# Kernel tuning notes

Hardware: AMD Instinct MI355X
Metric: run time of the kernel (lower is better)

Reference implementation:

```python
import jax, jax.numpy as jnp
import numpy as np

LN_EPS = 1e-5


def setup_inputs() -> dict:
    key = jax.random.key(0)
    k1, k2, k3 = jax.random.split(key, 3)
    B, L, D = 8, 2048, 512
    K, Dc = 8192, 16
    x = jax.random.normal(k1, (B, L, D), dtype=jnp.float32)
    # xavier_uniform for Linear(dim -> codebook_dim), weight shape (Dc, D)
    bound = float(np.sqrt(6.0 / (D + Dc)))
    proj_weight = jax.random.uniform(k2, (Dc, D), dtype=jnp.float32, minval=-bound, maxval=bound)
    codebook = jax.random.normal(k3, (K, Dc), dtype=jnp.float32)
    return {"x": x, "proj_weight": proj_weight, "codebook": codebook}


def reference(x, proj_weight, codebook):
    # random projection: (B,L,D) @ (D,Dc) -> (B,L,Dc)
    h = jnp.einsum("bld,cd->blc", x, proj_weight)
    # LayerNorm over last dim, no affine params
    mu = jnp.mean(h, axis=-1, keepdims=True)
    var = jnp.mean(jnp.square(h - mu), axis=-1, keepdims=True)
    h = (h - mu) / jnp.sqrt(var + LN_EPS)
    # squared-distance via dot-product decomposition; avoids (B,L,K,Dc) blowup.
    # argmin of ||h - c||^2 == argmin of ||h - c|| (sqrt is monotone).
    h2 = jnp.sum(jnp.square(h), axis=-1, keepdims=True)        # (B,L,1)
    c2 = jnp.sum(jnp.square(codebook), axis=-1)                # (K,)
    dots = jnp.einsum("blc,kc->blk", h, codebook)              # (B,L,K)
    dist2 = h2 - 2.0 * dots + c2                               # (B,L,K)
    codes = jnp.argmin(dist2, axis=-1)                         # (B,L) int
    return codes
```

## Files before the change

kernel.cpp:

```cpp
#include <hip/hip_runtime.h>
#include <math.h>

#define LN_EPS 1e-5f

typedef _Float16 f16;
typedef _Float16 f16x8 __attribute__((ext_vector_type(8)));
typedef _Float16 f16x2 __attribute__((ext_vector_type(2)));
typedef float f32x4 __attribute__((ext_vector_type(4)));

constexpr int DC = 16;
constexpr int K = 8192;
constexpr int NTOK = 16384;
constexpr int D = 512;
constexpr float SCALE = 16384.f;
constexpr float EPS_S = LN_EPS * SCALE * SCALE;

static __device__ __forceinline__ f16x8 mk8(f16x2 a, f16x2 b, f16x2 c,
                                            f16x2 d) {
  union {
    f16x2 p[4];
    f16x8 v;
  } u;
  u.p[0] = a;
  u.p[1] = b;
  u.p[2] = c;
  u.p[3] = d;
  return u.v;
}

static __device__ __forceinline__ void hilo2(float f0, float f1, f16x2& ph,
                                             f16x2& pl) {
  float h0 = __uint_as_float(__float_as_uint(f0) & 0xFFFFE000u);
  float h1 = __uint_as_float(__float_as_uint(f1) & 0xFFFFE000u);
  ph = __builtin_bit_cast(f16x2, __builtin_amdgcn_cvt_pkrtz(h0, h1));
  pl = __builtin_bit_cast(f16x2,
                          __builtin_amdgcn_cvt_pkrtz(f0 - h0, f1 - h1));
}

__global__ __launch_bounds__(256) void prep(const float* __restrict__ cb,
                                            const float* __restrict__ wq,
                                            f16* __restrict__ cbA,
                                            float* __restrict__ c2s,
                                            f16* __restrict__ wAf) {
  const int tid = threadIdx.x;

  if (blockIdx.x == K / 64) {
#pragma unroll
    for (int i = 0; i < 8; ++i) {
      int slot = tid + 256 * i;
      int tile = slot >> 6;
      int l = slot & 63;
      int g = l >> 4;
      int col = l & 15;
      int doff = (g & 1) * 8;
      const float* wp = wq + (size_t)col * D + tile * 16 + doff;
      f32x4 u0 = *(const f32x4*)wp;
      f32x4 u1 = *(const f32x4*)(wp + 4);
      f16x2 ph[4], pl[4];
      hilo2(u0[0] * 64.f, u0[1] * 64.f, ph[0], pl[0]);
      hilo2(u0[2] * 64.f, u0[3] * 64.f, ph[1], pl[1]);
      hilo2(u1[0] * 64.f, u1[1] * 64.f, ph[2], pl[2]);
      hilo2(u1[2] * 64.f, u1[3] * 64.f, ph[3], pl[3]);
      f16x8 hi = mk8(ph[0], ph[1], ph[2], ph[3]);
      f16x8 lo = mk8(pl[0], pl[1], pl[2], pl[3]);
      *(f16x8*)(wAf + (size_t)slot * 8) = (g < 2) ? hi : lo;
    }
    return;
  }

  const int ti = tid >> 6;
  const int l = tid & 63;
  const int ct = blockIdx.x * 4 + ti;
  const int code = ct * 16 + (l & 15);
  const int g = l >> 4;

  const float* row = cb + (size_t)code * DC + (g & 1) * 8;
  f32x4 v0 = *(const f32x4*)row;
  f32x4 v1 = *(const f32x4*)(row + 4);
  f16x2 ph[4], pl[4];
  hilo2(v0[0] * -128.f, v0[1] * -128.f, ph[0], pl[0]);
  hilo2(v0[2] * -128.f, v0[3] * -128.f, ph[1], pl[1]);
  hilo2(v1[0] * -128.f, v1[1] * -128.f, ph[2], pl[2]);
  hilo2(v1[2] * -128.f, v1[3] * -128.f, ph[3], pl[3]);
  f16x8 hi = mk8(ph[0], ph[1], ph[2], ph[3]);
  f16x8 lo = mk8(pl[0], pl[1], pl[2], pl[3]);
  *(f16x8*)(cbA + ((size_t)ct * 64 + l) * 8) = (g < 2) ? hi : lo;

  if (g == 0) {
    const f32x4* rw = (const f32x4*)(cb + (size_t)code * DC);
    f32x4 a0 = rw[0], a1 = rw[1], a2 = rw[2], a3 = rw[3];
    float s = 0.f;
#pragma unroll
    for (int p = 0; p < 4; ++p)
      s += a0[p] * a0[p] + a1[p] * a1[p] + a2[p] * a2[p] + a3[p] * a3[p];
    c2s[code] = (s + 16.5f) * SCALE;
  }
}

__global__ __launch_bounds__(1024, 8) void fused(
    const float* __restrict__ x, const float* __restrict__ cb,
    const f16* __restrict__ cbA, const float* __restrict__ c2s,
    const f16* __restrict__ wAf, int* __restrict__ out) {
  __shared__ float comb[16 * 16 * 20];
  __shared__ float hsm[32 * 20];
  __shared__ float fin_d[16][32];
  __shared__ int fin_t[16][32];

  const int tid = threadIdx.x;
  const int w = tid >> 6;
  const int lane = tid & 63;
  const int g = lane >> 4;
  const int col = lane & 15;
  const int doff = (g & 1) * 8;
  const int tb = blockIdx.x * 32;

  const int j = w & 1;
  const int dq8 = w >> 1;

  const float* xrow = x + (size_t)(tb + j * 16 + col) * D + dq8 * 64 + doff;
  f32x4 xu0[4], xu1[4];
#pragma unroll
  for (int st = 0; st < 4; ++st) {
    xu0[st] = *(const f32x4*)(xrow + st * 16);
    xu1[st] = *(const f32x4*)(xrow + st * 16 + 4);
  }
  f16x8 aw[4];
#pragma unroll
  for (int st = 0; st < 4; ++st)
    aw[st] = *(const f16x8*)(wAf + ((size_t)(dq8 * 4 + st) * 64 + lane) * 8);

  f32x4 acc = {0.f, 0.f, 0.f, 0.f};
#pragma unroll
  for (int st = 0; st < 4; ++st) {
    f16x2 ph[4], pl[4];
    hilo2(xu0[st][0] * 256.f, xu0[st][1] * 256.f, ph[0], pl[0]);
    hilo2(xu0[st][2] * 256.f, xu0[st][3] * 256.f, ph[1], pl[1]);
    hilo2(xu1[st][0] * 256.f, xu1[st][1] * 256.f, ph[2], pl[2]);
    hilo2(xu1[st][2] * 256.f, xu1[st][3] * 256.f, ph[3], pl[3]);
    f16x8 bh = mk8(ph[0], ph[1], ph[2], ph[3]);
    f16x8 bl = mk8(pl[0], pl[1], pl[2], pl[3]);
    f16x8 b1 = (g < 2) ? bh : bl;
    f16x8 b2 = (g < 2) ? bl : bh;
    acc = __builtin_amdgcn_mfma_f32_16x16x32_f16(aw[st], b1, acc, 0, 0, 0);
    acc = __builtin_amdgcn_mfma_f32_16x16x32_f16(aw[st], b2, acc, 0, 0, 0);
  }
  *(f32x4*)&comb[(w * 16 + col) * 20 + g * 4] = acc;
  __syncthreads();

  if (tid < 512) {
    const int tokL = tid >> 4;
    const int cL = tid & 15;
    const int jL = tokL >> 4;
    const int colL = tokL & 15;
    float hv = 0.f;
#pragma unroll
    for (int dq = 0; dq < 8; ++dq)
      hv += comb[((dq * 2 + jL) * 16 + colL) * 20 + cL];
    float s = hv;
    s += __shfl_xor(s, 1, 16);
    s += __shfl_xor(s, 2, 16);
    s += __shfl_xor(s, 4, 16);
    s += __shfl_xor(s, 8, 16);
    float mu = s * (1.f / 16.f);
    float diff = hv - mu;
    float v2 = diff * diff;
    v2 += __shfl_xor(v2, 1, 16);
    v2 += __shfl_xor(v2, 2, 16);
    v2 += __shfl_xor(v2, 4, 16);
    v2 += __shfl_xor(v2, 8, 16);
    float var = v2 * (1.f / 16.f);
    hsm[tokL * 20 + cL] = diff / sqrtf(var + EPS_S);
  }
  __syncthreads();

  f16x8 b1[2], b2[2];
#pragma unroll
  for (int jj = 0; jj < 2; ++jj) {
    const float* hp = &hsm[(jj * 16 + col) * 20 + doff];
    f32x4 u0 = *(const f32x4*)hp;
    f32x4 u1 = *(const f32x4*)(hp + 4);
    f16x2 ph[4], pl[4];
    hilo2(u0[0] * 256.f, u0[1] * 256.f, ph[0], pl[0]);
    hilo2(u0[2] * 256.f, u0[3] * 256.f, ph[1], pl[1]);
    hilo2(u1[0] * 256.f, u1[1] * 256.f, ph[2], pl[2]);
    hilo2(u1[2] * 256.f, u1[3] * 256.f, ph[3], pl[3]);
    f16x8 bh = mk8(ph[0], ph[1], ph[2], ph[3]);
    f16x8 bl = mk8(pl[0], pl[1], pl[2], pl[3]);
    b1[jj] = (g < 2) ? bh : bl;
    b2[jj] = (g < 2) ? bl : bh;
  }

  const int q = w;
  float best0 = 3.0e38f, best1 = 3.0e38f;
  int grp0 = 0, grp1 = 0;
  const f16* pa = cbA + ((size_t)q * 32 * 64 + lane) * 8;
  const float* pc = c2s + q * 512 + g * 4;

  for (int gi = 0; gi < 4; ++gi) {
    float sb0 = best0, sb1 = best1;
#pragma unroll
    for (int ti = 0; ti < 8; ++ti) {
      int t = gi * 8 + ti;
      f16x8 a = *(const f16x8*)(pa + (size_t)t * 512);
      f32x4 c2v = *(const f32x4*)(pc + t * 16);
      __builtin_amdgcn_s_setprio(1);
      f32x4 a0 = __builtin_amdgcn_mfma_f32_16x16x32_f16(a, b1[0], c2v, 0, 0, 0);
      a0 = __builtin_amdgcn_mfma_f32_16x16x32_f16(a, b2[0], a0, 0, 0, 0);
      f32x4 a1 = __builtin_amdgcn_mfma_f32_16x16x32_f16(a, b1[1], c2v, 0, 0, 0);
      a1 = __builtin_amdgcn_mfma_f32_16x16x32_f16(a, b2[1], a1, 0, 0, 0);
      __builtin_amdgcn_s_setprio(0);
      best0 = fminf(best0, fminf(fminf(a0[0], a0[1]), fminf(a0[2], a0[3])));
      best1 = fminf(best1, fminf(fminf(a1[0], a1[1]), fminf(a1[2], a1[3])));
    }
    grp0 = (best0 < sb0) ? gi : grp0;
    grp1 = (best1 < sb1) ? gi : grp1;
  }

  int tg0 = grp0 * 4 + g, tg1 = grp1 * 4 + g;
#pragma unroll
  for (int off = 16; off <= 32; off <<= 1) {
    float od = __shfl_xor(best0, off);
    int ot = __shfl_xor(tg0, off);
    bool tk = (od < best0) || (od == best0 && ot < tg0);
    best0 = tk ? od : best0;
    tg0 = tk ? ot : tg0;
    od = __shfl_xor(best1, off);
    ot = __shfl_xor(tg1, off);
    tk = (od < best1) || (od == best1 && ot < tg1);
    best1 = tk ? od : best1;
    tg1 = tk ? ot : tg1;
  }
  if (lane < 16) {
    fin_d[q][lane] = best0;
    fin_t[q][lane] = tg0;
    fin_d[q][16 + lane] = best1;
    fin_t[q][16 + lane] = tg1;
  }
  __syncthreads();

  if (tid < 512) {
    const int tok = tid >> 4;
    const int c = tid & 15;
    float bd = fin_d[0][tok];
    int btag = fin_t[0][tok];
    int bq = 0;
#pragma unroll
    for (int q2 = 1; q2 < 16; ++q2) {
      float d2 = fin_d[q2][tok];
      int t2 = fin_t[q2][tok];
      bool tk = d2 < bd;
      bd = tk ? d2 : bd;
      btag = tk ? t2 : btag;
      bq = tk ? q2 : bq;
    }
    const int kb = bq * 512 + (btag >> 2) * 128 + (btag & 3) * 4;

    f32x4 h0 = *(const f32x4*)&hsm[tok * 20];
    f32x4 h1 = *(const f32x4*)&hsm[tok * 20 + 4];
    f32x4 h2 = *(const f32x4*)&hsm[tok * 20 + 8];
    f32x4 h3 = *(const f32x4*)&hsm[tok * 20 + 12];

    float bestd = 3.0e38f;
    int bestk = kb;
#pragma unroll
    for (int e2 = 0; e2 < 2; ++e2) {
      int e = c * 2 + e2;
      int kk = kb + (e >> 2) * 16 + (e & 3);
      const f32x4* cr = (const f32x4*)(cb + (size_t)kk * DC);
      f32x4 c0 = cr[0], c1 = cr[1], c2r = cr[2], c3 = cr[3];
      float sd = 0.f;
#pragma unroll
      for (int p = 0; p < 4; ++p) {
        float d0 = h0[p] - c0[p];
        float d1 = h1[p] - c1[p];
        float dd2 = h2[p] - c2r[p];
        float d3 = h3[p] - c3[p];
        sd = fmaf(d0, d0, sd);
        sd = fmaf(d1, d1, sd);
        sd = fmaf(dd2, dd2, sd);
        sd = fmaf(d3, d3, sd);
      }
      bool tk = sd < bestd;
      bestd = tk ? sd : bestd;
      bestk = tk ? kk : bestk;
    }
#pragma unroll
    for (int off = 1; off < 16; off <<= 1) {
      float od = __shfl_xor(bestd, off, 16);
      int ok = __shfl_xor(bestk, off, 16);
      bool tk = (od < bestd) || (od == bestd && ok < bestk);
      bestd = tk ? od : bestd;
      bestk = tk ? ok : bestk;
    }
    if (c == 0) out[tb + tok] = bestk;
  }
}

extern "C" void kernel_launch(void* const* d_in, const int* in_sizes, int n_in,
                              void* d_out, int out_size, void* d_ws,
                              size_t ws_size, hipStream_t stream) {
  const float* x = (const float*)d_in[0];
  const float* w = (const float*)d_in[1];
  const float* cb = (const float*)d_in[2];

  f16* cbA = (f16*)d_ws;
  float* c2s = (float*)(cbA + (size_t)K * 32);
  f16* wAf = (f16*)(c2s + K);

  prep<<<K / 64 + 1, 256, 0, stream>>>(cb, w, cbA, c2s, wAf);
  fused<<<NTOK / 32, 1024, 0, stream>>>(x, cb, cbA, c2s, wAf, (int*)d_out);
}
```

Baseline: 40.50 us.

## Process 64 tokens per block so each codebook fragment feeds four token tiles

Doubles the tokens per block from 32 to 64. Each wave now applies every loaded codebook fragment and c2 vector to four 16-token tiles instead of two, which halves codebook traffic per token and the grid size. The projection stage is reorganised to 4 token groups by 4 D-quarters with loads inside the loop, and all 1024 threads now take part in layernorm and the refinement. In exchange it uses more registers per thread, lowers the launch-bounds occupancy hint, and leaves 256 blocks for the whole device.

```diff
diff --git a/kernel.cpp b/kernel.cpp
--- a/kernel.cpp
+++ b/kernel.cpp
@@ -97,14 +97,14 @@
   }
 }
 
-__global__ __launch_bounds__(1024, 8) void fused(
+__global__ __launch_bounds__(1024, 4) void fused(
     const float* __restrict__ x, const float* __restrict__ cb,
     const f16* __restrict__ cbA, const float* __restrict__ c2s,
     const f16* __restrict__ wAf, int* __restrict__ out) {
   __shared__ float comb[16 * 16 * 20];
-  __shared__ float hsm[32 * 20];
-  __shared__ float fin_d[16][32];
-  __shared__ int fin_t[16][32];
+  __shared__ float hsm[64 * 20];
+  __shared__ float fin_d[16][64];
+  __shared__ int fin_t[16][64];
 
   const int tid = threadIdx.x;
   const int w = tid >> 6;
@@ -112,50 +112,43 @@
   const int g = lane >> 4;
   const int col = lane & 15;
   const int doff = (g & 1) * 8;
-  const int tb = blockIdx.x * 32;
-
-  const int j = w & 1;
-  const int dq8 = w >> 1;
-
-  const float* xrow = x + (size_t)(tb + j * 16 + col) * D + dq8 * 64 + doff;
-  f32x4 xu0[4], xu1[4];
-#pragma unroll
-  for (int st = 0; st < 4; ++st) {
-    xu0[st] = *(const f32x4*)(xrow + st * 16);
-    xu1[st] = *(const f32x4*)(xrow + st * 16 + 4);
-  }
-  f16x8 aw[4];
-#pragma unroll
-  for (int st = 0; st < 4; ++st)
-    aw[st] = *(const f16x8*)(wAf + ((size_t)(dq8 * 4 + st) * 64 + lane) * 8);
-
+  const int tb = blockIdx.x * 64;
+
+  const int j = w & 3;
+  const int dq = w >> 2;
+
+  const float* xrow = x + (size_t)(tb + j * 16 + col) * D + dq * 128 + doff;
   f32x4 acc = {0.f, 0.f, 0.f, 0.f};
 #pragma unroll
-  for (int st = 0; st < 4; ++st) {
+  for (int st = 0; st < 8; ++st) {
+    f16x8 aw =
+        *(const f16x8*)(wAf + ((size_t)(dq * 8 + st) * 64 + lane) * 8);
+    f32x4 u0 = *(const f32x4*)(xrow + st * 16);
+    f32x4 u1 = *(const f32x4*)(xrow + st * 16 + 4);
     f16x2 ph[4], pl[4];
-    hilo2(xu0[st][0] * 256.f, xu0[st][1] * 256.f, ph[0], pl[0]);
-    hilo2(xu0[st][2] * 256.f, xu0[st][3] * 256.f, ph[1], pl[1]);
-    hilo2(xu1[st][0] * 256.f, xu1[st][1] * 256.f, ph[2], pl[2]);
-    hilo2(xu1[st][2] * 256.f, xu1[st][3] * 256.f, ph[3], pl[3]);
+    hilo2(u0[0] * 256.f, u0[1] * 256.f, ph[0], pl[0]);
+    hilo2(u0[2] * 256.f, u0[3] * 256.f, ph[1], pl[1]);
+    hilo2(u1[0] * 256.f, u1[1] * 256.f, ph[2], pl[2]);
+    hilo2(u1[2] * 256.f, u1[3] * 256.f, ph[3], pl[3]);
     f16x8 bh = mk8(ph[0], ph[1], ph[2], ph[3]);
     f16x8 bl = mk8(pl[0], pl[1], pl[2], pl[3]);
     f16x8 b1 = (g < 2) ? bh : bl;
     f16x8 b2 = (g < 2) ? bl : bh;
-    acc = __builtin_amdgcn_mfma_f32_16x16x32_f16(aw[st], b1, acc, 0, 0, 0);
-    acc = __builtin_amdgcn_mfma_f32_16x16x32_f16(aw[st], b2, acc, 0, 0, 0);
+    acc = __builtin_amdgcn_mfma_f32_16x16x32_f16(aw, b1, acc, 0, 0, 0);
+    acc = __builtin_amdgcn_mfma_f32_16x16x32_f16(aw, b2, acc, 0, 0, 0);
   }
   *(f32x4*)&comb[(w * 16 + col) * 20 + g * 4] = acc;
   __syncthreads();
 
-  if (tid < 512) {
+  {
     const int tokL = tid >> 4;
     const int cL = tid & 15;
     const int jL = tokL >> 4;
     const int colL = tokL & 15;
     float hv = 0.f;
 #pragma unroll
-    for (int dq = 0; dq < 8; ++dq)
-      hv += comb[((dq * 2 + jL) * 16 + colL) * 20 + cL];
+    for (int dq2 = 0; dq2 < 4; ++dq2)
+      hv += comb[((dq2 * 4 + jL) * 16 + colL) * 20 + cL];
     float s = hv;
     s += __shfl_xor(s, 1, 16);
     s += __shfl_xor(s, 2, 16);
@@ -173,9 +166,9 @@
   }
   __syncthreads();
 
-  f16x8 b1[2], b2[2];
-#pragma unroll
-  for (int jj = 0; jj < 2; ++jj) {
+  f16x8 b1[4], b2[4];
+#pragma unroll
+  for (int jj = 0; jj < 4; ++jj) {
     const float* hp = &hsm[(jj * 16 + col) * 20 + doff];
     f32x4 u0 = *(const f32x4*)hp;
     f32x4 u1 = *(const f32x4*)(hp + 4);
@@ -191,54 +184,59 @@
   }
 
   const int q = w;
-  float best0 = 3.0e38f, best1 = 3.0e38f;
-  int grp0 = 0, grp1 = 0;
+  float best[4] = {3.0e38f, 3.0e38f, 3.0e38f, 3.0e38f};
+  int grp[4] = {0, 0, 0, 0};
   const f16* pa = cbA + ((size_t)q * 32 * 64 + lane) * 8;
   const float* pc = c2s + q * 512 + g * 4;
 
   for (int gi = 0; gi < 4; ++gi) {
-    float sb0 = best0, sb1 = best1;
+    float sb0 = best[0], sb1 = best[1], sb2 = best[2], sb3 = best[3];
 #pragma unroll
     for (int ti = 0; ti < 8; ++ti) {
       int t = gi * 8 + ti;
       f16x8 a = *(const f16x8*)(pa + (size_t)t * 512);
       f32x4 c2v = *(const f32x4*)(pc + t * 16);
       __builtin_amdgcn_s_setprio(1);
-      f32x4 a0 = __builtin_amdgcn_mfma_f32_16x16x32_f16(a, b1[0], c2v, 0, 0, 0);
-      a0 = __builtin_amdgcn_mfma_f32_16x16x32_f16(a, b2[0], a0, 0, 0, 0);
-      f32x4 a1 = __builtin_amdgcn_mfma_f32_16x16x32_f16(a, b1[1], c2v, 0, 0, 0);
-      a1 = __builtin_amdgcn_mfma_f32_16x16x32_f16(a, b2[1], a1, 0, 0, 0);
+      f32x4 d0 = __builtin_amdgcn_mfma_f32_16x16x32_f16(a, b1[0], c2v, 0, 0, 0);
+      d0 = __builtin_amdgcn_mfma_f32_16x16x32_f16(a, b2[0], d0, 0, 0, 0);
+      f32x4 d1 = __builtin_amdgcn_mfma_f32_16x16x32_f16(a, b1[1], c2v, 0, 0, 0);
+      d1 = __builtin_amdgcn_mfma_f32_16x16x32_f16(a, b2[1], d1, 0, 0, 0);
+      f32x4 d2 = __builtin_amdgcn_mfma_f32_16x16x32_f16(a, b1[2], c2v, 0, 0, 0);
+      d2 = __builtin_amdgcn_mfma_f32_16x16x32_f16(a, b2[2], d2, 0, 0, 0);
+      f32x4 d3 = __builtin_amdgcn_mfma_f32_16x16x32_f16(a, b1[3], c2v, 0, 0, 0);
+      d3 = __builtin_amdgcn_mfma_f32_16x16x32_f16(a, b2[3], d3, 0, 0, 0);
       __builtin_amdgcn_s_setprio(0);
-      best0 = fminf(best0, fminf(fminf(a0[0], a0[1]), fminf(a0[2], a0[3])));
-      best1 = fminf(best1, fminf(fminf(a1[0], a1[1]), fminf(a1[2], a1[3])));
-    }
-    grp0 = (best0 < sb0) ? gi : grp0;
-    grp1 = (best1 < sb1) ? gi : grp1;
-  }
-
-  int tg0 = grp0 * 4 + g, tg1 = grp1 * 4 + g;
-#pragma unroll
-  for (int off = 16; off <= 32; off <<= 1) {
-    float od = __shfl_xor(best0, off);
-    int ot = __shfl_xor(tg0, off);
-    bool tk = (od < best0) || (od == best0 && ot < tg0);
-    best0 = tk ? od : best0;
-    tg0 = tk ? ot : tg0;
-    od = __shfl_xor(best1, off);
-    ot = __shfl_xor(tg1, off);
-    tk = (od < best1) || (od == best1 && ot < tg1);
-    best1 = tk ? od : best1;
-    tg1 = tk ? ot : tg1;
-  }
-  if (lane < 16) {
-    fin_d[q][lane] = best0;
-    fin_t[q][lane] = tg0;
-    fin_d[q][16 + lane] = best1;
-    fin_t[q][16 + lane] = tg1;
+      best[0] = fminf(best[0], fminf(fminf(d0[0], d0[1]), fminf(d0[2], d0[3])));
+      best[1] = fminf(best[1], fminf(fminf(d1[0], d1[1]), fminf(d1[2], d1[3])));
+      best[2] = fminf(best[2], fminf(fminf(d2[0], d2[1]), fminf(d2[2], d2[3])));
+      best[3] = fminf(best[3], fminf(fminf(d3[0], d3[1]), fminf(d3[2], d3[3])));
+    }
+    grp[0] = (best[0] < sb0) ? gi : grp[0];
+    grp[1] = (best[1] < sb1) ? gi : grp[1];
+    grp[2] = (best[2] < sb2) ? gi : grp[2];
+    grp[3] = (best[3] < sb3) ? gi : grp[3];
+  }
+
+#pragma unroll
+  for (int jj = 0; jj < 4; ++jj) {
+    float d = best[jj];
+    int tg = grp[jj] * 4 + g;
+#pragma unroll
+    for (int off = 16; off <= 32; off <<= 1) {
+      float od = __shfl_xor(d, off);
+      int ot = __shfl_xor(tg, off);
+      bool tk = (od < d) || (od == d && ot < tg);
+      d = tk ? od : d;
+      tg = tk ? ot : tg;
+    }
+    if (lane < 16) {
+      fin_d[q][jj * 16 + lane] = d;
+      fin_t[q][jj * 16 + lane] = tg;
+    }
   }
   __syncthreads();
 
-  if (tid < 512) {
+  {
     const int tok = tid >> 4;
     const int c = tid & 15;
     float bd = fin_d[0][tok];
@@ -271,14 +269,14 @@
       float sd = 0.f;
 #pragma unroll
       for (int p = 0; p < 4; ++p) {
-        float d0 = h0[p] - c0[p];
-        float d1 = h1[p] - c1[p];
-        float dd2 = h2[p] - c2r[p];
-        float d3 = h3[p] - c3[p];
-        sd = fmaf(d0, d0, sd);
-        sd = fmaf(d1, d1, sd);
-        sd = fmaf(dd2, dd2, sd);
-        sd = fmaf(d3, d3, sd);
+        float e0 = h0[p] - c0[p];
+        float e1 = h1[p] - c1[p];
+        float e2f = h2[p] - c2r[p];
+        float e3 = h3[p] - c3[p];
+        sd = fmaf(e0, e0, sd);
+        sd = fmaf(e1, e1, sd);
+        sd = fmaf(e2f, e2f, sd);
+        sd = fmaf(e3, e3, sd);
       }
       bool tk = sd < bestd;
       bestd = tk ? sd : bestd;
@@ -308,5 +306,5 @@
   f16* wAf = (f16*)(c2s + K);
 
   prep<<<K / 64 + 1, 256, 0, stream>>>(cb, w, cbA, c2s, wAf);
-  fused<<<NTOK / 32, 1024, 0, stream>>>(x, cb, cbA, c2s, wAf, (int*)d_out);
-}
+  fused<<<NTOK / 64, 1024, 0, stream>>>(x, cb, cbA, c2s, wAf, (int*)d_out);
+}
```

After: 39.58 us, median of 2. -2.3%, faster.
